# Optimization experiments

Hardware: AMD Instinct MI355X
Metric: run time of the kernel (lower is better)

Reference implementation:

```python
import jax, jax.numpy as jnp
import numpy as np

H_DIM = 4096
N_HEADS = 4
D_HEAD = H_DIM // N_HEADS  # 1024; also forced to equal the node count N
N = D_HEAD
LN_EPS = 1e-5


def setup_inputs() -> dict:
    key = jax.random.key(0)
    ks = jax.random.split(key, 10)
    s = 0.02
    return {
        "node1": jax.random.normal(ks[0], (N, H_DIM), dtype=jnp.float32),
        "node2": jax.random.normal(ks[1], (N, H_DIM), dtype=jnp.float32),
        # stacked per-head projection weights (torch Linear y = x @ W^T + b; here W stored as [h, in, out])
        "Wq": jax.random.normal(ks[2], (N_HEADS, H_DIM, D_HEAD), dtype=jnp.float32) * s,
        "bq": jax.random.normal(ks[3], (N_HEADS, D_HEAD), dtype=jnp.float32) * s,
        "Wk": jax.random.normal(ks[4], (N_HEADS, H_DIM, D_HEAD), dtype=jnp.float32) * s,
        "bk": jax.random.normal(ks[5], (N_HEADS, D_HEAD), dtype=jnp.float32) * s,
        "Wv": jax.random.normal(ks[6], (N_HEADS, H_DIM, D_HEAD), dtype=jnp.float32) * s,
        "bv": jax.random.normal(ks[7], (N_HEADS, D_HEAD), dtype=jnp.float32) * s,
        "gamma": jnp.ones((H_DIM,), dtype=jnp.float32),
        "beta": jnp.zeros((H_DIM,), dtype=jnp.float32),
    }


def reference(node1, node2, Wq, bq, Wk, bk, Wv, bv, gamma, beta):
    # per-head projections: [h, N, d]
    q = jnp.einsum('nd,hdf->hnf', node1, Wq) + bq[:, None, :]
    k = jnp.einsum('md,hdf->hmf', node2, Wk) + bk[:, None, :]
    v = jnp.einsum('md,hdf->hmf', node2, Wv) + bv[:, None, :]
    scale = 1.0 / jnp.sqrt(jnp.asarray(D_HEAD, dtype=q.dtype))
    # scores [h, N, N]; elementwise-multiplied by v (no softmax). Valid because N == D_HEAD.
    r = (jnp.einsum('hnf,hmf->hnm', q, k) * scale) * v
    # concat heads along last dim: [N, h * d] = [N, H_DIM]
    out = jnp.transpose(r, (1, 0, 2)).reshape(N, H_DIM)
    # LayerNorm over last dim (biased variance, matching torch)
    mu = jnp.mean(out, axis=-1, keepdims=True)
    var = jnp.mean((out - mu) ** 2, axis=-1, keepdims=True)
    return (out - mu) * jax.lax.rsqrt(var + LN_EPS) * gamma + beta
```

## Files before the change

### kernel.cpp

```cpp
#include <hip/hip_runtime.h>

#define H_DIM 4096
#define NHEADS 4
#define DH 1024
#define NROWS 1024

typedef __attribute__((ext_vector_type(8))) short short8;
typedef __attribute__((ext_vector_type(4))) short short4v;
typedef __attribute__((ext_vector_type(4))) float f32x4;

__device__ __forceinline__ short f2bf(float f) {
  union { float f; unsigned u; } v; v.f = f;
  unsigned r = v.u + 0x7fffu + ((v.u >> 16) & 1u);
  return (short)(r >> 16);
}
__device__ __forceinline__ float bf2f(short s) {
  union { unsigned u; float f; } v;
  v.u = ((unsigned)(unsigned short)s) << 16;
  return v.f;
}

__launch_bounds__(256, 2)
__global__ void qkv_gemm(const float* __restrict__ node1,
                         const float* __restrict__ node2,
                         const float* __restrict__ Wq, const float* __restrict__ bq,
                         const float* __restrict__ Wk, const float* __restrict__ bk,
                         const float* __restrict__ Wv, const float* __restrict__ bv,
                         short* __restrict__ qkv_out) {
  const int gid = blockIdx.x;
  const int gemm = gid >> 6;
  const int tile = gid & 63;
  const int qkv = gemm >> 2;
  const int h = gemm & 3;
  const float* A = (qkv == 0) ? node1 : node2;
  const float* W = (qkv == 0) ? Wq : (qkv == 1 ? Wk : Wv);
  const float* bias = (qkv == 0) ? bq : (qkv == 1 ? bk : bv);
  const float* B = W + (size_t)h * H_DIM * DH;
  const float* bh = bias + h * DH;
  short* C = qkv_out + (size_t)gemm * NROWS * DH;

  const int bm0 = (tile >> 3) * 128;
  const int bn0 = (tile & 7) * 128;

  __shared__ short As[128][40];
  __shared__ short Bs[128][40];

  const int t = threadIdx.x;
  const int lane = t & 63;
  const int w = t >> 6;
  const int wm = (w >> 1) * 64;
  const int wn = (w & 1) * 64;
  const int lr = lane & 15;
  const int lk = lane >> 4;

  const int ar = t >> 3;
  const int ac = (t & 7) * 4;
  const int bfc = t & 127;
  const int bd = (t >> 7) * 16;

  f32x4 acc[4][4];
#pragma unroll
  for (int m = 0; m < 4; ++m)
#pragma unroll
    for (int n = 0; n < 4; ++n)
      acc[m][n] = (f32x4)(0.0f);

  f32x4 rA[4];
  float rB[16];

  const float* Abase = A + (size_t)bm0 * H_DIM;
  const float* Bbase = B + bn0 + bfc;

#pragma unroll
  for (int p = 0; p < 4; ++p)
    rA[p] = *(const f32x4*)&Abase[(size_t)(ar + 32 * p) * H_DIM + ac];
#pragma unroll
  for (int i = 0; i < 16; ++i)
    rB[i] = Bbase[(size_t)(bd + i) * DH];

  const int NKT = H_DIM / 32;
  for (int kt = 0; kt < NKT; ++kt) {
    __syncthreads();
#pragma unroll
    for (int p = 0; p < 4; ++p) {
      short4v s;
      s.x = f2bf(rA[p].x); s.y = f2bf(rA[p].y);
      s.z = f2bf(rA[p].z); s.w = f2bf(rA[p].w);
      *(short4v*)&As[ar + 32 * p][ac] = s;
    }
    {
      short8 lo, hi;
#pragma unroll
      for (int i = 0; i < 8; ++i) { lo[i] = f2bf(rB[i]); hi[i] = f2bf(rB[8 + i]); }
      *(short8*)&Bs[bfc][bd] = lo;
      *(short8*)&Bs[bfc][bd + 8] = hi;
    }
    __syncthreads();
    if (kt + 1 < NKT) {
      const int k0 = (kt + 1) * 32;
#pragma unroll
      for (int p = 0; p < 4; ++p)
        rA[p] = *(const f32x4*)&Abase[(size_t)(ar + 32 * p) * H_DIM + k0 + ac];
#pragma unroll
      for (int i = 0; i < 16; ++i)
        rB[i] = Bbase[(size_t)(k0 + bd + i) * DH];
    }
    short8 af[4], bf_[4];
#pragma unroll
    for (int m = 0; m < 4; ++m)
      af[m] = *(const short8*)&As[wm + m * 16 + lr][lk * 8];
#pragma unroll
    for (int n = 0; n < 4; ++n)
      bf_[n] = *(const short8*)&Bs[wn + n * 16 + lr][lk * 8];
#pragma unroll
    for (int m = 0; m < 4; ++m)
#pragma unroll
      for (int n = 0; n < 4; ++n)
        acc[m][n] = __builtin_amdgcn_mfma_f32_16x16x32_bf16(af[m], bf_[n], acc[m][n], 0, 0, 0);
  }

#pragma unroll
  for (int n = 0; n < 4; ++n) {
    const int col = bn0 + wn + n * 16 + lr;
    const float bv_ = bh[col];
#pragma unroll
    for (int m = 0; m < 4; ++m) {
      const int row0 = bm0 + wm + m * 16 + lk * 4;
#pragma unroll
      for (int r = 0; r < 4; ++r)
        C[(size_t)(row0 + r) * DH + col] = f2bf(acc[m][n][r] + bv_);
    }
  }
}

__launch_bounds__(256, 2)
__global__ void attn_gemm(const short* __restrict__ qb, const short* __restrict__ kb,
                          const short* __restrict__ vb, float* __restrict__ out) {
  const int gid = blockIdx.x;
  const int h = gid >> 6;
  const int tile = gid & 63;
  const int bm0 = (tile >> 3) * 128;
  const int bn0 = (tile & 7) * 128;
  const short* Q = qb + (size_t)h * NROWS * DH;
  const short* K = kb + (size_t)h * NROWS * DH;
  const short* V = vb + (size_t)h * NROWS * DH;

  __shared__ short As[128][40];
  __shared__ short Bs[128][40];

  const int t = threadIdx.x;
  const int lane = t & 63;
  const int w = t >> 6;
  const int wm = (w >> 1) * 64;
  const int wn = (w & 1) * 64;
  const int lr = lane & 15;
  const int lk = lane >> 4;

  const int sr = t >> 2;
  const int sc = (t & 3) * 8;

  f32x4 acc[4][4];
#pragma unroll
  for (int m = 0; m < 4; ++m)
#pragma unroll
    for (int n = 0; n < 4; ++n)
      acc[m][n] = (f32x4)(0.0f);

  short8 rA[2], rB[2];
#pragma unroll
  for (int p = 0; p < 2; ++p) {
    rA[p] = *(const short8*)&Q[(size_t)(bm0 + sr + 64 * p) * DH + sc];
    rB[p] = *(const short8*)&K[(size_t)(bn0 + sr + 64 * p) * DH + sc];
  }

  const int NKT = DH / 32;
  for (int kt = 0; kt < NKT; ++kt) {
    __syncthreads();
#pragma unroll
    for (int p = 0; p < 2; ++p) {
      *(short8*)&As[sr + 64 * p][sc] = rA[p];
      *(short8*)&Bs[sr + 64 * p][sc] = rB[p];
    }
    __syncthreads();
    if (kt + 1 < NKT) {
      const int k0 = (kt + 1) * 32;
#pragma unroll
      for (int p = 0; p < 2; ++p) {
        rA[p] = *(const short8*)&Q[(size_t)(bm0 + sr + 64 * p) * DH + k0 + sc];
        rB[p] = *(const short8*)&K[(size_t)(bn0 + sr + 64 * p) * DH + k0 + sc];
      }
    }
    short8 af[4], bf_[4];
#pragma unroll
    for (int m = 0; m < 4; ++m)
      af[m] = *(const short8*)&As[wm + m * 16 + lr][lk * 8];
#pragma unroll
    for (int n = 0; n < 4; ++n)
      bf_[n] = *(const short8*)&Bs[wn + n * 16 + lr][lk * 8];
#pragma unroll
    for (int m = 0; m < 4; ++m)
#pragma unroll
      for (int n = 0; n < 4; ++n)
        acc[m][n] = __builtin_amdgcn_mfma_f32_16x16x32_bf16(af[m], bf_[n], acc[m][n], 0, 0, 0);
  }

  const float scale = 0.03125f;
#pragma unroll
  for (int n = 0; n < 4; ++n) {
    const int col = bn0 + wn + n * 16 + lr;
#pragma unroll
    for (int m = 0; m < 4; ++m) {
      const int row0 = bm0 + wm + m * 16 + lk * 4;
#pragma unroll
      for (int r = 0; r < 4; ++r) {
        const int row = row0 + r;
        const float vv = bf2f(V[(size_t)row * DH + col]);
        out[(size_t)row * H_DIM + h * DH + col] = acc[m][n][r] * scale * vv;
      }
    }
  }
}

__launch_bounds__(256, 4)
__global__ void ln_kernel(float* __restrict__ out, const float* __restrict__ gamma,
                          const float* __restrict__ beta) {
  const int row = blockIdx.x;
  const int t = threadIdx.x;
  float* p = out + (size_t)row * H_DIM;
  f32x4 x[4];
  float s1 = 0.f, s2 = 0.f;
#pragma unroll
  for (int i = 0; i < 4; ++i) {
    x[i] = *(const f32x4*)&p[t * 4 + i * 1024];
    s1 += x[i].x + x[i].y + x[i].z + x[i].w;
    s2 += x[i].x * x[i].x + x[i].y * x[i].y + x[i].z * x[i].z + x[i].w * x[i].w;
  }
#pragma unroll
  for (int o = 32; o > 0; o >>= 1) {
    s1 += __shfl_down(s1, o);
    s2 += __shfl_down(s2, o);
  }
  __shared__ float w1[4], w2[4];
  if ((t & 63) == 0) { w1[t >> 6] = s1; w2[t >> 6] = s2; }
  __syncthreads();
  const float tot1 = w1[0] + w1[1] + w1[2] + w1[3];
  const float tot2 = w2[0] + w2[1] + w2[2] + w2[3];
  const float mu = tot1 * (1.0f / H_DIM);
  const float var = tot2 * (1.0f / H_DIM) - mu * mu;
  const float rs = rsqrtf(var + 1e-5f);
#pragma unroll
  for (int i = 0; i < 4; ++i) {
    const int c = t * 4 + i * 1024;
    const f32x4 g = *(const f32x4*)&gamma[c];
    const f32x4 b = *(const f32x4*)&beta[c];
    f32x4 y;
    y.x = (x[i].x - mu) * rs * g.x + b.x;
    y.y = (x[i].y - mu) * rs * g.y + b.y;
    y.z = (x[i].z - mu) * rs * g.z + b.z;
    y.w = (x[i].w - mu) * rs * g.w + b.w;
    *(f32x4*)&p[c] = y;
  }
}

extern "C" void kernel_launch(void* const* d_in, const int* in_sizes, int n_in,
                              void* d_out, int out_size, void* d_ws, size_t ws_size,
                              hipStream_t stream) {
  const float* node1 = (const float*)d_in[0];
  const float* node2 = (const float*)d_in[1];
  const float* Wq = (const float*)d_in[2];
  const float* bq = (const float*)d_in[3];
  const float* Wk = (const float*)d_in[4];
  const float* bk = (const float*)d_in[5];
  const float* Wv = (const float*)d_in[6];
  const float* bv = (const float*)d_in[7];
  const float* gamma = (const float*)d_in[8];
  const float* beta = (const float*)d_in[9];
  float* out = (float*)d_out;

  short* qkv = (short*)d_ws;
  short* qb = qkv;
  short* kb = qkv + (size_t)4 * 1024 * 1024;
  short* vb = qkv + (size_t)8 * 1024 * 1024;

  qkv_gemm<<<768, 256, 0, stream>>>(node1, node2, Wq, bq, Wk, bk, Wv, bv, qkv);
  attn_gemm<<<256, 256, 0, stream>>>(qb, kb, vb, out);
  ln_kernel<<<1024, 256, 0, stream>>>(out, gamma, beta);
}
```

Measured before the change: 230.6 us.

## Pre-convert inputs to bf16 and use async global-to-LDS loads in GEMMs

Adds pre-pass kernels that convert the node matrices to bf16 and the weights to transposed bf16 in workspace. New GEMM kernels use global_load_lds direct-to-LDS copies with double buffering instead of register staging, and the attention GEMM is replaced by the same design. This is meant to remove per-tile fp32-to-bf16 conversion and strided weight loads from the hot loop. The cost is extra conversion passes over roughly 200MB of fp32 weights each call, plus a dependence on workspace size, with a fallback path when the workspace is too small.

```diff
diff --git a/kernel.cpp b/kernel.cpp
--- a/kernel.cpp
+++ b/kernel.cpp
@@ -1,13 +1,15 @@
 #include <hip/hip_runtime.h>
 
 #define H_DIM 4096
-#define NHEADS 4
 #define DH 1024
 #define NROWS 1024
 
 typedef __attribute__((ext_vector_type(8))) short short8;
 typedef __attribute__((ext_vector_type(4))) short short4v;
 typedef __attribute__((ext_vector_type(4))) float f32x4;
+
+#define AS_GLOBAL __attribute__((address_space(1)))
+#define AS_LDS __attribute__((address_space(3)))
 
 __device__ __forceinline__ short f2bf(float f) {
   union { float f; unsigned u; } v; v.f = f;
@@ -18,6 +20,216 @@
   union { unsigned u; float f; } v;
   v.u = ((unsigned)(unsigned short)s) << 16;
   return v.f;
+}
+
+__device__ __forceinline__ void gload16(const void* g, void* l) {
+  __builtin_amdgcn_global_load_lds((const AS_GLOBAL void*)g, (AS_LDS void*)l, 16, 0, 0);
+}
+
+__device__ __forceinline__ void stage_tile(const short* Xrow0, size_t rowstride, int kbase,
+                                           short* lds, int t) {
+  const int w = t >> 6;
+#pragma unroll
+  for (int p = 0; p < 2; ++p) {
+    const short* g = Xrow0 + (size_t)(p * 64 + (t >> 2)) * rowstride + kbase + (t & 3) * 8;
+    char* l = (char*)lds + p * 4096 + w * 1024;
+    gload16(g, l);
+  }
+}
+
+__global__ void convert_nodes(const float* __restrict__ n1, const float* __restrict__ n2,
+                              short* __restrict__ o1, short* __restrict__ o2) {
+  const float* src = blockIdx.y ? n2 : n1;
+  short* dst = blockIdx.y ? o2 : o1;
+  const size_t i = ((size_t)blockIdx.x * 256 + threadIdx.x) * 8;
+  f32x4 a = *(const f32x4*)&src[i];
+  f32x4 b = *(const f32x4*)&src[i + 4];
+  short8 s;
+  s[0] = f2bf(a.x); s[1] = f2bf(a.y); s[2] = f2bf(a.z); s[3] = f2bf(a.w);
+  s[4] = f2bf(b.x); s[5] = f2bf(b.y); s[6] = f2bf(b.z); s[7] = f2bf(b.w);
+  *(short8*)&dst[i] = s;
+}
+
+__global__ void convert_w_t(const float* __restrict__ W, short* __restrict__ Wt) {
+  __shared__ short tile[64][72];
+  const int h = blockIdx.z, dt = blockIdx.y, ft = blockIdx.x;
+  const float* Wh = W + (size_t)h * H_DIM * DH;
+  short* Wth = Wt + (size_t)h * DH * H_DIM;
+  const int t = threadIdx.x;
+  {
+    const int d = t >> 2, f0 = (t & 3) * 16;
+    const float* src = Wh + (size_t)(dt * 64 + d) * DH + ft * 64 + f0;
+    f32x4 v0 = *(const f32x4*)(src + 0);
+    f32x4 v1 = *(const f32x4*)(src + 4);
+    f32x4 v2 = *(const f32x4*)(src + 8);
+    f32x4 v3 = *(const f32x4*)(src + 12);
+    short8 s0, s1;
+    s0[0] = f2bf(v0.x); s0[1] = f2bf(v0.y); s0[2] = f2bf(v0.z); s0[3] = f2bf(v0.w);
+    s0[4] = f2bf(v1.x); s0[5] = f2bf(v1.y); s0[6] = f2bf(v1.z); s0[7] = f2bf(v1.w);
+    s1[0] = f2bf(v2.x); s1[1] = f2bf(v2.y); s1[2] = f2bf(v2.z); s1[3] = f2bf(v2.w);
+    s1[4] = f2bf(v3.x); s1[5] = f2bf(v3.y); s1[6] = f2bf(v3.z); s1[7] = f2bf(v3.w);
+    *(short8*)&tile[d][f0] = s0;
+    *(short8*)&tile[d][f0 + 8] = s1;
+  }
+  __syncthreads();
+  {
+    const int f = t >> 2, d0 = (t & 3) * 16;
+    short8 o0, o1;
+#pragma unroll
+    for (int j = 0; j < 8; ++j) o0[j] = tile[d0 + j][f];
+#pragma unroll
+    for (int j = 0; j < 8; ++j) o1[j] = tile[d0 + 8 + j][f];
+    short* dst = Wth + (size_t)(ft * 64 + f) * H_DIM + dt * 64 + d0;
+    *(short8*)(dst) = o0;
+    *(short8*)(dst + 8) = o1;
+  }
+}
+
+__launch_bounds__(256)
+__global__ void qkv_bt(const short* __restrict__ n1b, const short* __restrict__ n2b,
+                       const short* __restrict__ Wt,
+                       const float* __restrict__ bq, const float* __restrict__ bk,
+                       const float* __restrict__ bv,
+                       short* __restrict__ qkv_out, int g0) {
+  const int bid = blockIdx.x;
+  const int gl = bid >> 6;
+  const int gg = g0 + gl;
+  const int tile = bid & 63;
+  const short* A = (gg < 4) ? n1b : n2b;
+  const short* B = Wt + (size_t)gl * NROWS * H_DIM;
+  const float* bias = ((gg < 4) ? bq : (gg < 8) ? bk : bv) + (gg & 3) * DH;
+  short* C = qkv_out + (size_t)gg * NROWS * DH;
+  const int bm0 = (tile >> 3) * 128, bn0 = (tile & 7) * 128;
+
+  __shared__ short As[2][4096];
+  __shared__ short Bs[2][4096];
+
+  const int t = threadIdx.x;
+  const int lane = t & 63, w = t >> 6;
+  const int wm = (w >> 1) * 64, wn = (w & 1) * 64;
+  const int lr = lane & 15, lk = lane >> 4;
+
+  const short* Arow0 = A + (size_t)bm0 * H_DIM;
+  const short* Brow0 = B + (size_t)bn0 * H_DIM;
+
+  f32x4 acc[4][4];
+#pragma unroll
+  for (int m = 0; m < 4; ++m)
+#pragma unroll
+    for (int n = 0; n < 4; ++n)
+      acc[m][n] = (f32x4)(0.0f);
+
+  stage_tile(Arow0, H_DIM, 0, &As[0][0], t);
+  stage_tile(Brow0, H_DIM, 0, &Bs[0][0], t);
+  __syncthreads();
+
+  const int NKT = H_DIM / 32;
+  int cur = 0;
+  for (int kt = 0; kt < NKT; ++kt) {
+    if (kt + 1 < NKT) {
+      stage_tile(Arow0, H_DIM, (kt + 1) * 32, &As[cur ^ 1][0], t);
+      stage_tile(Brow0, H_DIM, (kt + 1) * 32, &Bs[cur ^ 1][0], t);
+    }
+    short8 af[4], bf_[4];
+#pragma unroll
+    for (int m = 0; m < 4; ++m)
+      af[m] = *(const short8*)((const char*)&As[cur][0] + (wm + m * 16 + lr) * 64 + lk * 16);
+#pragma unroll
+    for (int n = 0; n < 4; ++n)
+      bf_[n] = *(const short8*)((const char*)&Bs[cur][0] + (wn + n * 16 + lr) * 64 + lk * 16);
+#pragma unroll
+    for (int m = 0; m < 4; ++m)
+#pragma unroll
+      for (int n = 0; n < 4; ++n)
+        acc[m][n] = __builtin_amdgcn_mfma_f32_16x16x32_bf16(af[m], bf_[n], acc[m][n], 0, 0, 0);
+    __syncthreads();
+    cur ^= 1;
+  }
+
+#pragma unroll
+  for (int n = 0; n < 4; ++n) {
+    const int col = bn0 + wn + n * 16 + lr;
+    const float bv_ = bias[col];
+#pragma unroll
+    for (int m = 0; m < 4; ++m) {
+      const int row0 = bm0 + wm + m * 16 + lk * 4;
+#pragma unroll
+      for (int r = 0; r < 4; ++r)
+        C[(size_t)(row0 + r) * DH + col] = f2bf(acc[m][n][r] + bv_);
+    }
+  }
+}
+
+__launch_bounds__(256)
+__global__ void attn_bt(const short* __restrict__ qkv, float* __restrict__ out) {
+  const int bid = blockIdx.x;
+  const int h = bid >> 6;
+  const int tile = bid & 63;
+  const short* Q = qkv + (size_t)h * NROWS * DH;
+  const short* K = qkv + (size_t)(4 + h) * NROWS * DH;
+  const short* V = qkv + (size_t)(8 + h) * NROWS * DH;
+  const int bm0 = (tile >> 3) * 128, bn0 = (tile & 7) * 128;
+
+  __shared__ short As[2][4096];
+  __shared__ short Bs[2][4096];
+
+  const int t = threadIdx.x;
+  const int lane = t & 63, w = t >> 6;
+  const int wm = (w >> 1) * 64, wn = (w & 1) * 64;
+  const int lr = lane & 15, lk = lane >> 4;
+
+  const short* Arow0 = Q + (size_t)bm0 * DH;
+  const short* Brow0 = K + (size_t)bn0 * DH;
+
+  f32x4 acc[4][4];
+#pragma unroll
+  for (int m = 0; m < 4; ++m)
+#pragma unroll
+    for (int n = 0; n < 4; ++n)
+      acc[m][n] = (f32x4)(0.0f);
+
+  stage_tile(Arow0, DH, 0, &As[0][0], t);
+  stage_tile(Brow0, DH, 0, &Bs[0][0], t);
+  __syncthreads();
+
+  const int NKT = DH / 32;
+  int cur = 0;
+  for (int kt = 0; kt < NKT; ++kt) {
+    if (kt + 1 < NKT) {
+      stage_tile(Arow0, DH, (kt + 1) * 32, &As[cur ^ 1][0], t);
+      stage_tile(Brow0, DH, (kt + 1) * 32, &Bs[cur ^ 1][0], t);
+    }
+    short8 af[4], bf_[4];
+#pragma unroll
+    for (int m = 0; m < 4; ++m)
+      af[m] = *(const short8*)((const char*)&As[cur][0] + (wm + m * 16 + lr) * 64 + lk * 16);
+#pragma unroll
+    for (int n = 0; n < 4; ++n)
+      bf_[n] = *(const short8*)((const char*)&Bs[cur][0] + (wn + n * 16 + lr) * 64 + lk * 16);
+#pragma unroll
+    for (int m = 0; m < 4; ++m)
+#pragma unroll
+      for (int n = 0; n < 4; ++n)
+        acc[m][n] = __builtin_amdgcn_mfma_f32_16x16x32_bf16(af[m], bf_[n], acc[m][n], 0, 0, 0);
+    __syncthreads();
+    cur ^= 1;
+  }
+
+  const float scale = 0.03125f;
+#pragma unroll
+  for (int n = 0; n < 4; ++n) {
+    const int col = bn0 + wn + n * 16 + lr;
+#pragma unroll
+    for (int m = 0; m < 4; ++m) {
+      const int row0 = bm0 + wm + m * 16 + lk * 4;
+#pragma unroll
+      for (int r = 0; r < 4; ++r) {
+        const int row = row0 + r;
+        const float vv = bf2f(V[(size_t)row * DH + col]);
+        out[(size_t)row * H_DIM + h * DH + col] = acc[m][n][r] * scale * vv;
+      }
+    }
+  }
 }
 
 __launch_bounds__(256, 2)
@@ -38,13 +250,10 @@
   const float* B = W + (size_t)h * H_DIM * DH;
   const float* bh = bias + h * DH;
   short* C = qkv_out + (size_t)gemm * NROWS * DH;
-
   const int bm0 = (tile >> 3) * 128;
   const int bn0 = (tile & 7) * 128;
-
   __shared__ short As[128][40];
   __shared__ short Bs[128][40];
-
   const int t = threadIdx.x;
   const int lane = t & 63;
   const int w = t >> 6;
@@ -52,32 +261,26 @@
   const int wn = (w & 1) * 64;
   const int lr = lane & 15;
   const int lk = lane >> 4;
-
   const int ar = t >> 3;
   const int ac = (t & 7) * 4;
   const int bfc = t & 127;
   const int bd = (t >> 7) * 16;
-
   f32x4 acc[4][4];
 #pragma unroll
   for (int m = 0; m < 4; ++m)
 #pragma unroll
     for (int n = 0; n < 4; ++n)
       acc[m][n] = (f32x4)(0.0f);
-
   f32x4 rA[4];
   float rB[16];
-
   const float* Abase = A + (size_t)bm0 * H_DIM;
   const float* Bbase = B + bn0 + bfc;
-
 #pragma unroll
   for (int p = 0; p < 4; ++p)
     rA[p] = *(const f32x4*)&Abase[(size_t)(ar + 32 * p) * H_DIM + ac];
 #pragma unroll
   for (int i = 0; i < 16; ++i)
     rB[i] = Bbase[(size_t)(bd + i) * DH];
-
   const int NKT = H_DIM / 32;
   for (int kt = 0; kt < NKT; ++kt) {
     __syncthreads();
@@ -118,7 +321,6 @@
       for (int n = 0; n < 4; ++n)
         acc[m][n] = __builtin_amdgcn_mfma_f32_16x16x32_bf16(af[m], bf_[n], acc[m][n], 0, 0, 0);
   }
-
 #pragma unroll
   for (int n = 0; n < 4; ++n) {
     const int col = bn0 + wn + n * 16 + lr;
@@ -129,94 +331,6 @@
 #pragma unroll
       for (int r = 0; r < 4; ++r)
         C[(size_t)(row0 + r) * DH + col] = f2bf(acc[m][n][r] + bv_);
-    }
-  }
-}
-
-__launch_bounds__(256, 2)
-__global__ void attn_gemm(const short* __restrict__ qb, const short* __restrict__ kb,
-                          const short* __restrict__ vb, float* __restrict__ out) {
-  const int gid = blockIdx.x;
-  const int h = gid >> 6;
-  const int tile = gid & 63;
-  const int bm0 = (tile >> 3) * 128;
-  const int bn0 = (tile & 7) * 128;
-  const short* Q = qb + (size_t)h * NROWS * DH;
-  const short* K = kb + (size_t)h * NROWS * DH;
-  const short* V = vb + (size_t)h * NROWS * DH;
-
-  __shared__ short As[128][40];
-  __shared__ short Bs[128][40];
-
-  const int t = threadIdx.x;
-  const int lane = t & 63;
-  const int w = t >> 6;
-  const int wm = (w >> 1) * 64;
-  const int wn = (w & 1) * 64;
-  const int lr = lane & 15;
-  const int lk = lane >> 4;
-
-  const int sr = t >> 2;
-  const int sc = (t & 3) * 8;
-
-  f32x4 acc[4][4];
-#pragma unroll
-  for (int m = 0; m < 4; ++m)
-#pragma unroll
-    for (int n = 0; n < 4; ++n)
-      acc[m][n] = (f32x4)(0.0f);
-
-  short8 rA[2], rB[2];
-#pragma unroll
-  for (int p = 0; p < 2; ++p) {
-    rA[p] = *(const short8*)&Q[(size_t)(bm0 + sr + 64 * p) * DH + sc];
-    rB[p] = *(const short8*)&K[(size_t)(bn0 + sr + 64 * p) * DH + sc];
-  }
-
-  const int NKT = DH / 32;
-  for (int kt = 0; kt < NKT; ++kt) {
-    __syncthreads();
-#pragma unroll
-    for (int p = 0; p < 2; ++p) {
-      *(short8*)&As[sr + 64 * p][sc] = rA[p];
-      *(short8*)&Bs[sr + 64 * p][sc] = rB[p];
-    }
-    __syncthreads();
-    if (kt + 1 < NKT) {
-      const int k0 = (kt + 1) * 32;
-#pragma unroll
-      for (int p = 0; p < 2; ++p) {
-        rA[p] = *(const short8*)&Q[(size_t)(bm0 + sr + 64 * p) * DH + k0 + sc];
-        rB[p] = *(const short8*)&K[(size_t)(bn0 + sr + 64 * p) * DH + k0 + sc];
-      }
-    }
-    short8 af[4], bf_[4];
-#pragma unroll
-    for (int m = 0; m < 4; ++m)
-      af[m] = *(const short8*)&As[wm + m * 16 + lr][lk * 8];
-#pragma unroll
-    for (int n = 0; n < 4; ++n)
-      bf_[n] = *(const short8*)&Bs[wn + n * 16 + lr][lk * 8];
-#pragma unroll
-    for (int m = 0; m < 4; ++m)
-#pragma unroll
-      for (int n = 0; n < 4; ++n)
-        acc[m][n] = __builtin_amdgcn_mfma_f32_16x16x32_bf16(af[m], bf_[n], acc[m][n], 0, 0, 0);
-  }
-
-  const float scale = 0.03125f;
-#pragma unroll
-  for (int n = 0; n < 4; ++n) {
-    const int col = bn0 + wn + n * 16 + lr;
-#pragma unroll
-    for (int m = 0; m < 4; ++m) {
-      const int row0 = bm0 + wm + m * 16 + lk * 4;
-#pragma unroll
-      for (int r = 0; r < 4; ++r) {
-        const int row = row0 + r;
-        const float vv = bf2f(V[(size_t)row * DH + col]);
-        out[(size_t)row * H_DIM + h * DH + col] = acc[m][n][r] * scale * vv;
-      }
     }
   }
 }
@@ -277,12 +391,29 @@
   const float* beta = (const float*)d_in[9];
   float* out = (float*)d_out;
 
+  const size_t MB = (size_t)1 << 20;
   short* qkv = (short*)d_ws;
-  short* qb = qkv;
-  short* kb = qkv + (size_t)4 * 1024 * 1024;
-  short* vb = qkv + (size_t)8 * 1024 * 1024;
-
-  qkv_gemm<<<768, 256, 0, stream>>>(node1, node2, Wq, bq, Wk, bk, Wv, bv, qkv);
-  attn_gemm<<<256, 256, 0, stream>>>(qb, kb, vb, out);
+  short* n1b = qkv + ((size_t)12 << 20);
+  short* n2b = n1b + ((size_t)4 << 20);
+  short* Wt = qkv + ((size_t)20 << 20);
+
+  if (ws_size >= 136 * MB) {
+    convert_nodes<<<dim3(2048, 2), 256, 0, stream>>>(node1, node2, n1b, n2b);
+    convert_w_t<<<dim3(16, 64, 4), 256, 0, stream>>>(Wq, Wt);
+    convert_w_t<<<dim3(16, 64, 4), 256, 0, stream>>>(Wk, Wt + ((size_t)16 << 20));
+    convert_w_t<<<dim3(16, 64, 4), 256, 0, stream>>>(Wv, Wt + ((size_t)32 << 20));
+    qkv_bt<<<768, 256, 0, stream>>>(n1b, n2b, Wt, bq, bk, bv, qkv, 0);
+  } else if (ws_size >= 72 * MB) {
+    convert_nodes<<<dim3(2048, 2), 256, 0, stream>>>(node1, node2, n1b, n2b);
+    const float* Ws[3] = {Wq, Wk, Wv};
+    for (int s = 0; s < 3; ++s) {
+      convert_w_t<<<dim3(16, 64, 4), 256, 0, stream>>>(Ws[s], Wt);
+      qkv_bt<<<256, 256, 0, stream>>>(n1b, n2b, Wt, bq, bk, bv, qkv, s * 4);
+    }
+  } else {
+    qkv_gemm<<<768, 256, 0, stream>>>(node1, node2, Wq, bq, Wk, bk, Wv, bv, qkv);
+  }
+
+  attn_bt<<<256, 256, 0, stream>>>(qkv, out);
   ln_kernel<<<1024, 256, 0, stream>>>(out, gamma, beta);
 }
```

Result: slower. 237.6 us (+3.1%).
